# Kernel tuning notes

Measured on AMD Instinct MI355X. Metric: run time of the kernel, lower is better.

Reference implementation:

```python
import jax, jax.numpy as jnp
import numpy as np

THRESH = 1.0
TAU_M = 20.0
TAU_S = 5.0
NUM_STEPS = 16
SCALE = 0.3
BATCH = 128
DM = float(np.exp(-1.0 / TAU_M))  # membrane decay per step
DS = float(np.exp(-1.0 / TAU_S))  # synaptic decay per step


@jax.custom_vjp
def spike_fn(u):
    # Heaviside spike with rectangular surrogate gradient.
    return (u > 0.0).astype(u.dtype)

def _spike_fwd(u):
    return (u > 0.0).astype(u.dtype), u

def _spike_bwd(u, g):
    return (g * (jnp.abs(u) < 0.5).astype(u.dtype),)

spike_fn.defvjp(_spike_fwd, _spike_bwd)


def _conv(x, w):
    # 5x5, stride 1, pad 2, no bias (NCHW / OIHW)
    return jax.lax.conv_general_dilated(x, w, (1, 1), ((2, 2), (2, 2)),
                                        dimension_numbers=('NCHW', 'OIHW', 'NCHW'))


def _noso(op, x, sav, vm, vs):
    # NOSO dual-time-constant neuron: u = sav * (op(vm) - op(vs));
    # sav gates the neuron off after its single spike.
    vm = vm * DM + x
    vs = vs * DS + x
    um = op(vm)
    us = op(vs)
    u = sav * (um - us)
    spike = spike_fn(u - THRESH)
    sav = sav * (1.0 - spike)
    return sav, vm, vs, um, u, spike


def _min_pool(spike, latency):
    # latency-based 2x2/stride-2 min-pool: pass the spike of the
    # earliest-firing (minimum-latency) neuron in each window.
    B, C, H, W = spike.shape
    s = spike.reshape(B, C, H // 2, 2, W // 2, 2)
    l = latency.reshape(B, C, H // 2, 2, W // 2, 2)
    lmin = jnp.min(l, axis=(3, 5), keepdims=True)
    return jnp.max(s * (l == lmin).astype(s.dtype), axis=(3, 5))


def _fmnist_forward(inp, w_conv1, w_conv2, w_fc1, w_fc2):
    B = inp.shape[0]
    f32 = jnp.float32
    x = inp * SCALE
    z = lambda *s: jnp.zeros(s, f32)
    o = lambda *s: jnp.ones(s, f32)
    carry = (
        z(B, 1, 28, 28), z(B, 1, 28, 28),                      # input_u, in_spike
        z(B, 1, 28, 28), z(B, 1, 28, 28), o(B, 32, 28, 28),    # hc1_vm, hc1_vs, hc1_sav
        z(B, 32, 28, 28), NUM_STEPS * o(B, 32, 28, 28),        # p1_te, p1_lat
        z(B, 32, 14, 14), z(B, 32, 14, 14), o(B, 64, 14, 14),  # hc2_vm, hc2_vs, hc2_sav
        z(B, 64, 14, 14), NUM_STEPS * o(B, 64, 14, 14),        # p2_te, p2_lat
        z(B, 3136), z(B, 3136), o(B, 600),                     # hf1_vm, hf1_vs, hf1_sav
        z(B, 600), z(B, 600), o(B, 10),                        # hf2_vm, hf2_vs, hf2_sav
        NUM_STEPS * o(B, 10), z(B, 10), z(B, 10),              # out_t, out_u, t_elapse
        jnp.zeros(5, f32),                                     # sum_sp
    )

    def step(c, _):
        (input_u, in_spike, hc1_vm, hc1_vs, hc1_sav, p1_te, p1_lat,
         hc2_vm, hc2_vs, hc2_sav, p2_te, p2_lat,
         hf1_vm, hf1_vs, hf1_sav, hf2_vm, hf2_vs, hf2_sav,
         out_t, out_u, t_el, sum_sp) = c
        sg = jax.lax.stop_gradient
        # input encoding neuron (leaky integrator with reset-by-spike, thresh=1.0)
        input_u = input_u * DM * (1.0 - in_spike) + x
        in_spike = spike_fn(input_u - 1.0)
        # conv layer 1
        hc1_sav, hc1_vm, hc1_vs, hc1_um, _, hc1_spike = _noso(
            lambda v: _conv(v, w_conv1), in_spike, hc1_sav, hc1_vm, hc1_vs)
        p1_te = p1_te + sg(((p1_te + (hc1_um != 0).astype(jnp.float32)) != 0).astype(jnp.float32))
        p1_lat = p1_lat + sg(hc1_spike * (p1_te - NUM_STEPS + 1.0))
        # conv layer 2 on latency min-pooled spikes
        hc2_in = _min_pool(hc1_spike, sg(p1_lat))
        hc2_sav, hc2_vm, hc2_vs, hc2_um, _, hc2_spike = _noso(
            lambda v: _conv(v, w_conv2), hc2_in, hc2_sav, hc2_vm, hc2_vs)
        p2_te = p2_te + sg(((p2_te + (hc2_um != 0).astype(jnp.float32)) != 0).astype(jnp.float32))
        p2_lat = p2_lat + sg(hc2_spike * (p2_te - NUM_STEPS + 1.0))
        # fc layer 1
        hf1_in = _min_pool(hc2_spike, sg(p2_lat)).reshape(B, -1)
        hf1_sav, hf1_vm, hf1_vs, _, _, hf1_spike = _noso(
            lambda v: v @ w_fc1.T, hf1_in, hf1_sav, hf1_vm, hf1_vs)
        # output fc layer (outneuron=True: also exposes u)
        hf2_sav, hf2_vm, hf2_vs, _, hf2_u, hf2_spike = _noso(
            lambda v: v @ w_fc2.T, hf1_spike, hf2_sav, hf2_vm, hf2_vs)
        t_el = t_el + sg(((t_el + (hf2_u != 0).astype(jnp.float32)) != 0).astype(jnp.float32))
        out_t = out_t + hf2_spike * sg(t_el - NUM_STEPS)  # dodt forward: spike latency
        out_u = out_u + hf2_spike * hf2_u
        sum_sp = sum_sp + sg(jnp.stack([in_spike.sum(), hc1_spike.sum(), hc2_spike.sum(),
                                        hf1_spike.sum(), hf2_spike.sum()]))
        return (input_u, in_spike, hc1_vm, hc1_vs, hc1_sav, p1_te, p1_lat,
                hc2_vm, hc2_vs, hc2_sav, p2_te, p2_lat,
                hf1_vm, hf1_vs, hf1_sav, hf2_vm, hf2_vs, hf2_sav,
                out_t, out_u, t_el, sum_sp), None

    c, _ = jax.lax.scan(step, carry, None, length=NUM_STEPS)
    out_t, out_u, sum_sp = c[-4], c[-3], c[-1]
    return out_t, out_u, sum_sp


def _xavier(key, shape, fan_in, fan_out):
    bound = float(np.sqrt(6.0 / (fan_in + fan_out)))
    return jax.random.uniform(key, shape, jnp.float32, -bound, bound)


def setup_inputs() -> dict:
    key = jax.random.key(0)
    k0, k1, k2, k3, k4 = jax.random.split(key, 5)
    return {
        "input": jax.random.uniform(k0, (BATCH, 1, 28, 28), jnp.float32),
        "w_conv1": _xavier(k1, (32, 1, 5, 5), 1 * 25, 32 * 25),
        "w_conv2": _xavier(k2, (64, 32, 5, 5), 32 * 25, 64 * 25),
        "w_fc1": _xavier(k3, (600, 3136), 3136, 600),
        "w_fc2": _xavier(k4, (10, 600), 600, 10),
        "batch_size": BATCH,
    }


def reference(input, w_conv1, w_conv2, w_fc1, w_fc2, batch_size):
    return _fmnist_forward(input, w_conv1, w_conv2, w_fc1, w_fc2)
```

## Files before the change

### kernel.cpp

```cpp
#include <hip/hip_runtime.h>

#define BATCH 128

constexpr float DM = 0.95122942450071400910f;
constexpr float DS = 0.81873075307798185867f;

constexpr size_t o_wt   = 0;
constexpr size_t o_inb  = o_wt  + (size_t)3136 * 600;
constexpr size_t o_p1b  = o_inb + (size_t)16 * 128 * 32;
constexpr size_t o_flag = o_p1b + (size_t)16 * 128 * 32 * 18;
constexpr size_t o_p2m  = o_flag + 2048;
constexpr size_t o_c1   = o_p2m + 200704;
constexpr size_t TOTALF = o_c1 + (size_t)16 * 128 * 600 + 16;

__device__ __forceinline__ void block_sum_atomic(float v, float* red, float* dst) {
    int lane = threadIdx.x & 63;
    int wid  = threadIdx.x >> 6;
    #pragma unroll
    for (int o = 32; o; o >>= 1) v += __shfl_down(v, o, 64);
    if (lane == 0) red[wid] = v;
    __syncthreads();
    if (threadIdx.x == 0) {
        int nw = ((int)blockDim.x + 63) >> 6;
        float t = 0.f;
        for (int w = 0; w < nw; ++w) t += red[w];
        if (t != 0.f) atomicAdd(dst, t);
    }
    __syncthreads();
}

__global__ void k_transpose(const float* __restrict__ w, float* __restrict__ wt,
                            float* __restrict__ outz) {
    __shared__ float tile[32][33];
    int k0 = blockIdx.x * 32, j0 = blockIdx.y * 32;
    int lx = threadIdx.x & 31, ly = threadIdx.x >> 5;
    if (blockIdx.x == 0 && blockIdx.y == 0 && threadIdx.x < 5) outz[threadIdx.x] = 0.f;
    #pragma unroll
    for (int r = 0; r < 32; r += 8) {
        int j = j0 + ly + r, k = k0 + lx;
        tile[ly + r][lx] = (j < 600 && k < 3136) ? w[(size_t)j * 3136 + k] : 0.f;
    }
    __syncthreads();
    #pragma unroll
    for (int r = 0; r < 32; r += 8) {
        int k = k0 + ly + r, j = j0 + lx;
        if (k < 3136 && j < 600) wt[(size_t)k * 600 + j] = tile[lx][ly + r];
    }
}

__launch_bounds__(896)
__global__ void k_encode(const float* __restrict__ inp, unsigned* __restrict__ inb,
                         float* __restrict__ ssp) {
    __shared__ float red[16];
    int b = blockIdx.x, tid = threadIdx.x;
    int w = tid >> 6, lane = tid & 63;
    int r = lane >> 5, x = lane & 31;
    int y = 2 * w + r;
    float xv = (x < 28) ? inp[b * 784 + y * 28 + x] * 0.3f : 0.f;
    if (tid < 64) {
        int t = tid >> 2, rsel = tid & 3;
        inb[((size_t)t * 128 + b) * 32 + (rsel < 2 ? rsel : 28 + rsel)] = 0u;
    }
    float uin = 0.f, isp = 0.f, cnt = 0.f;
    for (int t = 0; t < 16; ++t) {
        uin = uin * DM * (1.f - isp) + xv;
        isp = (uin > 1.f && x < 28) ? 1.f : 0.f;
        cnt += isp;
        unsigned long long m = __ballot(isp != 0.f);
        if (lane == 0)       inb[((size_t)t * 128 + b) * 32 + (2 * w + 2)] = ((unsigned)m) << 2;
        else if (lane == 32) inb[((size_t)t * 128 + b) * 32 + (2 * w + 3)] = ((unsigned)(m >> 32)) << 2;
    }
    block_sum_atomic(cnt, red, &ssp[0]);
}

__launch_bounds__(256)
__global__ void k_conv1(const float* __restrict__ w1, const unsigned* __restrict__ inb,
                        unsigned* __restrict__ p1b, unsigned short* __restrict__ flags,
                        float* __restrict__ ssp) {
    __shared__ float2 lutA[320];
    __shared__ float2 lutB[320];
    __shared__ unsigned sib[512];
    __shared__ unsigned wor[8];
    __shared__ unsigned s_tm[4];
    __shared__ float red[4];
    int bo = blockIdx.x, b = bo >> 4, op = bo & 15;
    int oc0 = op * 2;
    int tid = threadIdx.x;
    int px = tid & 15, py = tid >> 4;
    bool pv = (px < 14) && (py < 14);
    int pb = (py < 14) ? 2 * py : 0;

    if (tid < 128) {
        int t = tid >> 3, k = tid & 7;
        int oc = oc0 + (k >> 2), rsel = k & 3;
        p1b[(((size_t)t * 128 + b) * 32 + oc) * 18 + (rsel < 2 ? rsel : 14 + rsel)] = 0u;
    }
    for (int e = tid; e < 320; e += 256) {
        int ky = e >> 6, m = e & 63;
        const float* wA = w1 + oc0 * 25 + ky * 5;
        float a0 = 0.f, a1 = 0.f, b0 = 0.f, b1 = 0.f;
        #pragma unroll
        for (int kx = 0; kx < 5; ++kx) {
            if ((m >> kx) & 1)       { a0 += wA[kx]; b0 += wA[25 + kx]; }
            if ((m >> (kx + 1)) & 1) { a1 += wA[kx]; b1 += wA[25 + kx]; }
        }
        lutA[e] = make_float2(a0, a1);
        lutB[e] = make_float2(b0, b1);
    }
    unsigned lb = 0;
    {
        unsigned w0 = inb[((size_t)(tid >> 5) * 128 + b) * 32 + (tid & 31)];
        unsigned w1v = inb[((size_t)((tid + 256) >> 5) * 128 + b) * 32 + (tid & 31)];
        sib[tid] = w0;
        sib[tid + 256] = w1v;
        if (w0)  lb |= 1u << (tid >> 5);
        if (w1v) lb |= 1u << ((tid >> 5) + 8);
    }
    #pragma unroll
    for (int off = 32; off; off >>= 1) lb |= __shfl_xor(lb, off, 64);
    if ((tid & 63) == 0) s_tm[tid >> 6] = lb;
    if (tid < 8) wor[tid] = 0u;
    __syncthreads();

    unsigned tmask = s_tm[0] | s_tm[1] | s_tm[2] | s_tm[3];
    unsigned smask = tmask;
    smask |= smask << 1; smask |= smask << 2; smask |= smask << 4; smask |= smask << 8;

    float umA[2][2] = {}, usA[2][2] = {}, teA[2][2] = {};
    float savA[2][2] = {{1.f,1.f},{1.f,1.f}}, ltA[2][2] = {{16.f,16.f},{16.f,16.f}};
    float umB[2][2] = {}, usB[2][2] = {}, teB[2][2] = {};
    float savB[2][2] = {{1.f,1.f},{1.f,1.f}}, ltB[2][2] = {{16.f,16.f},{16.f,16.f}};
    unsigned pmA = 0, pmB = 0;

    for (int t = 0; t < 16; ++t) {
        if (!((smask >> t) & 1u)) continue;
        unsigned rw[6];
        #pragma unroll
        for (int j = 0; j < 6; ++j) rw[j] = sib[t * 32 + pb + j];
        unsigned orall = rw[0] | rw[1] | rw[2] | rw[3] | rw[4] | rw[5];

        float cA[2][2] = {}, cB[2][2] = {};
        if (orall) {
            unsigned sh[6];
            #pragma unroll
            for (int j = 0; j < 6; ++j) sh[j] = (rw[j] >> (2 * px)) & 63u;
            #pragma unroll
            for (int r = 0; r < 2; ++r)
                #pragma unroll
                for (int ky = 0; ky < 5; ++ky) {
                    unsigned idx = ky * 64 + sh[r + ky];
                    float2 vA = lutA[idx];
                    float2 vB = lutB[idx];
                    cA[r][0] += vA.x; cA[r][1] += vA.y;
                    cB[r][0] += vB.x; cB[r][1] += vB.y;
                }
        }
        float sA[2][2], sB[2][2];
        #pragma unroll
        for (int r = 0; r < 2; ++r)
            #pragma unroll
            for (int cc = 0; cc < 2; ++cc) {
                umA[r][cc] = fmaf(umA[r][cc], DM, cA[r][cc]);
                usA[r][cc] = fmaf(usA[r][cc], DS, cA[r][cc]);
                float uA = savA[r][cc] * (umA[r][cc] - usA[r][cc]);
                bool fA = uA > 1.f;
                float a = fA ? 1.f : 0.f;
                savA[r][cc] = fA ? 0.f : savA[r][cc];
                teA[r][cc] += ((teA[r][cc] != 0.f) || (umA[r][cc] != 0.f)) ? 1.f : 0.f;
                ltA[r][cc] += a * (teA[r][cc] - 15.f);
                sA[r][cc] = a;
                umB[r][cc] = fmaf(umB[r][cc], DM, cB[r][cc]);
                usB[r][cc] = fmaf(usB[r][cc], DS, cB[r][cc]);
                float uB = savB[r][cc] * (umB[r][cc] - usB[r][cc]);
                bool fB = uB > 1.f;
                float bb = fB ? 1.f : 0.f;
                savB[r][cc] = fB ? 0.f : savB[r][cc];
                teB[r][cc] += ((teB[r][cc] != 0.f) || (umB[r][cc] != 0.f)) ? 1.f : 0.f;
                ltB[r][cc] += bb * (teB[r][cc] - 15.f);
                sB[r][cc] = bb;
            }
        float sany = sA[0][0] + sA[0][1] + sA[1][0] + sA[1][1]
                   + sB[0][0] + sB[0][1] + sB[1][0] + sB[1][1];
        if (!__any(pv && sany != 0.f)) continue;
        float lmA = fminf(fminf(ltA[0][0], ltA[0][1]), fminf(ltA[1][0], ltA[1][1]));
        float oA = fmaxf(fmaxf(ltA[0][0] == lmA ? sA[0][0] : 0.f, ltA[0][1] == lmA ? sA[0][1] : 0.f),
                         fmaxf(ltA[1][0] == lmA ? sA[1][0] : 0.f, ltA[1][1] == lmA ? sA[1][1] : 0.f));
        float lmB = fminf(fminf(ltB[0][0], ltB[0][1]), fminf(ltB[1][0], ltB[1][1]));
        float oB = fmaxf(fmaxf(ltB[0][0] == lmB ? sB[0][0] : 0.f, ltB[0][1] == lmB ? sB[0][1] : 0.f),
                         fmaxf(ltB[1][0] == lmB ? sB[1][0] : 0.f, ltB[1][1] == lmB ? sB[1][1] : 0.f));
        bool hitA = (oA != 0.f) && pv;
        bool hitB = (oB != 0.f) && pv;
        unsigned long long balA = __ballot(hitA);
        unsigned long long balB = __ballot(hitB);
        int k = tid & 63;
        if (k < 4) {
            int prow = (tid >> 6) * 4 + k;
            if (prow < 14) {
                unsigned wdA = ((unsigned)(balA >> (k * 16)) & 0x3FFFu) << 2;
                unsigned wdB = ((unsigned)(balB >> (k * 16)) & 0x3FFFu) << 2;
                p1b[(((size_t)t * 128 + b) * 32 + oc0)     * 18 + prow + 2] = wdA;
                p1b[(((size_t)t * 128 + b) * 32 + oc0 + 1) * 18 + prow + 2] = wdB;
            }
        }
        if (hitA) pmA |= 1u << t;
        if (hitB) pmB |= 1u << t;
    }

    unsigned pA = pmA, pB = pmB;
    #pragma unroll
    for (int off = 32; off; off >>= 1) {
        pA |= __shfl_xor(pA, off, 64);
        pB |= __shfl_xor(pB, off, 64);
    }
    if ((tid & 63) == 0) { wor[(tid >> 6) * 2] = pA; wor[(tid >> 6) * 2 + 1] = pB; }
    float cnt = 0.f;
    if (pv)
        cnt = 8.f - (savA[0][0] + savA[0][1] + savA[1][0] + savA[1][1]
                   + savB[0][0] + savB[0][1] + savB[1][0] + savB[1][1]);
    block_sum_atomic(cnt, red, &ssp[1]);
    if (tid == 0) {
        flags[b * 32 + oc0]     = (unsigned short)(wor[0] | wor[2] | wor[4] | wor[6]);
        flags[b * 32 + oc0 + 1] = (unsigned short)(wor[1] | wor[3] | wor[5] | wor[7]);
    }
}

__launch_bounds__(256)
__global__ void k_conv2(const float* __restrict__ w2, const unsigned* __restrict__ p1b,
                        const unsigned short* __restrict__ flags,
                        unsigned short* __restrict__ p2m, float* __restrict__ ssp) {
    __shared__ float2 lut2[5120];
    int bo = blockIdx.x, op = bo & 31, bq = bo >> 5;
    int oc0 = op * 2;
    int tid = threadIdx.x;
    int wv = tid >> 6, lane = tid & 63;
    int b = bq * 4 + wv;
    bool valid = lane < 49;
    int pr = valid ? (lane / 7) : 0;
    int pc = valid ? (lane - pr * 7) : 0;
    int y0 = 2 * pr, x0 = 2 * pc;

    for (int e = tid; e < 5120; e += 256) {
        int m = e & 31, icky = e >> 5;
        const float* wA = w2 + oc0 * 800 + icky * 5;
        float a = 0.f, c = 0.f;
        #pragma unroll
        for (int kx = 0; kx < 5; ++kx)
            if ((m >> kx) & 1) { a += wA[kx]; c += wA[800 + kx]; }
        lut2[e] = make_float2(a, c);
    }
    unsigned fl = flags[b * 32 + (lane & 31)];
    __syncthreads();

    float umA[2][2] = {}, usA[2][2] = {}, teA[2][2] = {};
    float savA[2][2] = {{1.f,1.f},{1.f,1.f}}, ltA[2][2] = {{16.f,16.f},{16.f,16.f}};
    float umB[2][2] = {}, usB[2][2] = {}, teB[2][2] = {};
    float savB[2][2] = {{1.f,1.f},{1.f,1.f}}, ltB[2][2] = {{16.f,16.f},{16.f,16.f}};
    unsigned pmA = 0, pmB = 0;
    bool started = false;

    for (int t = 0; t < 16; ++t) {
        unsigned actbm = (unsigned)__ballot(((fl >> t) & 1u) && (lane < 32));
        started = started || (actbm != 0);
        if (!started) continue;
        float cA[2][2] = {}, cB[2][2] = {};
        unsigned bm = actbm;
        while (bm) {
            int ic = __builtin_ctz(bm); bm &= bm - 1;
            const unsigned* rp = p1b + (((size_t)t * 128 + b) * 32 + ic) * 18 + y0;
            unsigned r0 = rp[0], r1 = rp[1], r2 = rp[2],
                     r3 = rp[3], r4 = rp[4], r5 = rp[5];
            unsigned orall = r0 | r1 | r2 | r3 | r4 | r5;
            if (!valid || ((orall >> x0) & 63u) == 0) continue;
            unsigned sh[6] = {r0 >> x0, r1 >> x0, r2 >> x0, r3 >> x0, r4 >> x0, r5 >> x0};
            int base = ic * 160;
            #pragma unroll
            for (int r = 0; r < 2; ++r)
                #pragma unroll
                for (int ky = 0; ky < 5; ++ky) {
                    unsigned s6 = sh[r + ky];
                    float2 v0 = lut2[base + ky * 32 + (s6 & 31u)];
                    float2 v1 = lut2[base + ky * 32 + ((s6 >> 1) & 31u)];
                    cA[r][0] += v0.x; cB[r][0] += v0.y;
                    cA[r][1] += v1.x; cB[r][1] += v1.y;
                }
        }
        float sA[2][2], sB[2][2];
        #pragma unroll
        for (int r = 0; r < 2; ++r)
            #pragma unroll
            for (int cc = 0; cc < 2; ++cc) {
                umA[r][cc] = fmaf(umA[r][cc], DM, cA[r][cc]);
                usA[r][cc] = fmaf(usA[r][cc], DS, cA[r][cc]);
                float uA = savA[r][cc] * (umA[r][cc] - usA[r][cc]);
                bool fA = uA > 1.f;
                float a = fA ? 1.f : 0.f;
                savA[r][cc] = fA ? 0.f : savA[r][cc];
                teA[r][cc] += ((teA[r][cc] != 0.f) || (umA[r][cc] != 0.f)) ? 1.f : 0.f;
                ltA[r][cc] += a * (teA[r][cc] - 15.f);
                sA[r][cc] = a;
                umB[r][cc] = fmaf(umB[r][cc], DM, cB[r][cc]);
                usB[r][cc] = fmaf(usB[r][cc], DS, cB[r][cc]);
                float uB = savB[r][cc] * (umB[r][cc] - usB[r][cc]);
                bool fB = uB > 1.f;
                float bb = fB ? 1.f : 0.f;
                savB[r][cc] = fB ? 0.f : savB[r][cc];
                teB[r][cc] += ((teB[r][cc] != 0.f) || (umB[r][cc] != 0.f)) ? 1.f : 0.f;
                ltB[r][cc] += bb * (teB[r][cc] - 15.f);
                sB[r][cc] = bb;
            }
        float sany = sA[0][0] + sA[0][1] + sA[1][0] + sA[1][1]
                   + sB[0][0] + sB[0][1] + sB[1][0] + sB[1][1];
        if (!__any(valid && sany != 0.f)) continue;
        float lmA = fminf(fminf(ltA[0][0], ltA[0][1]), fminf(ltA[1][0], ltA[1][1]));
        float oA = fmaxf(fmaxf(ltA[0][0] == lmA ? sA[0][0] : 0.f, ltA[0][1] == lmA ? sA[0][1] : 0.f),
                         fmaxf(ltA[1][0] == lmA ? sA[1][0] : 0.f, ltA[1][1] == lmA ? sA[1][1] : 0.f));
        float lmB = fminf(fminf(ltB[0][0], ltB[0][1]), fminf(ltB[1][0], ltB[1][1]));
        float oB = fmaxf(fmaxf(ltB[0][0] == lmB ? sB[0][0] : 0.f, ltB[0][1] == lmB ? sB[0][1] : 0.f),
                         fmaxf(ltB[1][0] == lmB ? sB[1][0] : 0.f, ltB[1][1] == lmB ? sB[1][1] : 0.f));
        if (valid && oA != 0.f) pmA |= 1u << t;
        if (valid && oB != 0.f) pmB |= 1u << t;
    }
    if (valid) {
        int pos = pr * 7 + pc;
        p2m[((size_t)b * 64 + oc0)     * 49 + pos] = (unsigned short)pmA;
        p2m[((size_t)b * 64 + oc0 + 1) * 49 + pos] = (unsigned short)pmB;
    }
    float cnt = 0.f;
    if (valid)
        cnt = 8.f - (savA[0][0] + savA[0][1] + savA[1][0] + savA[1][1]
                   + savB[0][0] + savB[0][1] + savB[1][0] + savB[1][1]);
    __syncthreads();
    block_sum_atomic(cnt, (float*)lut2, &ssp[2]);
}

__launch_bounds__(640)
__global__ void k_fc1pre(const float* __restrict__ wt, const unsigned short* __restrict__ p2m,
                         float* __restrict__ C1) {
    __shared__ unsigned short s_m[3136];
    __shared__ int s_idx[3136];
    __shared__ int s_nnz;
    int bt = blockIdx.x;
    int b = bt & 127, t = bt >> 7;
    int tid = threadIdx.x;

    for (int k = tid; k < 3136; k += 640) s_m[k] = p2m[(size_t)b * 3136 + k];
    __syncthreads();
    if (tid < 64) {
        int count = 0;
        for (int o = 0; o < 64; ++o) {
            unsigned v = (tid < 49) ? (unsigned)s_m[o * 49 + tid] : 0u;
            unsigned long long m = __ballot((v >> t) & 1u);
            if ((m >> tid) & 1ull)
                s_idx[count + __popcll(m & ((1ull << tid) - 1ull))] = o * 49 + tid;
            count += __popcll(m);
        }
        if (tid == 0) s_nnz = count;
    }
    __syncthreads();
    int nnz = s_nnz;

    if (tid < 600) {
        float a0 = 0.f, a1 = 0.f, a2 = 0.f, a3 = 0.f;
        int i = 0;
        for (; i + 4 <= nnz; i += 4) {
            a0 += wt[(size_t)s_idx[i]     * 600 + tid];
            a1 += wt[(size_t)s_idx[i + 1] * 600 + tid];
            a2 += wt[(size_t)s_idx[i + 2] * 600 + tid];
            a3 += wt[(size_t)s_idx[i + 3] * 600 + tid];
        }
        for (; i < nnz; ++i) a0 += wt[(size_t)s_idx[i] * 600 + tid];
        C1[(size_t)bt * 600 + tid] = (a0 + a1) + (a2 + a3);
    }
}

__launch_bounds__(640)
__global__ void k_fc12b(const float* __restrict__ C1, const float* __restrict__ wf2,
                        float* __restrict__ out) {
    __shared__ unsigned short s_m1[600];
    __shared__ float red[16];
    __shared__ float s_c2[10];
    int b = blockIdx.x, tid = threadIdx.x;
    int w = tid >> 6, lane = tid & 63;

    float cnt1 = 0.f;
    if (tid < 600) {
        float c[16];
        #pragma unroll
        for (int t = 0; t < 16; ++t) c[t] = C1[((size_t)t * 128 + b) * 600 + tid];
        float um = 0.f, us = 0.f, sv = 1.f;
        unsigned msk = 0;
        #pragma unroll
        for (int t = 0; t < 16; ++t) {
            um = fmaf(um, DM, c[t]);
            us = fmaf(us, DS, c[t]);
            float u = sv * (um - us);
            float s = (u > 1.f) ? 1.f : 0.f;
            sv *= (1.f - s);
            msk |= (s != 0.f) ? (1u << t) : 0u;
            cnt1 += s;
        }
        s_m1[tid] = (unsigned short)msk;
    }
    block_sum_atomic(cnt1, red, &out[2563]);

    const float* wrow = wf2 + w * 600;
    float wv[10]; unsigned mv[10];
    #pragma unroll
    for (int i = 0; i < 10; ++i) {
        int j = lane + i * 64;
        bool ok = (j < 600);
        wv[i] = ok ? wrow[j] : 0.f;
        mv[i] = ok ? (unsigned)s_m1[j] : 0u;
    }
    float f2um = 0.f, f2us = 0.f, f2sv = 1.f;
    float tel = 0.f, ot = 16.f, ou = 0.f, cnt2 = 0.f;
    for (int t = 0; t < 16; ++t) {
        float a = 0.f;
        #pragma unroll
        for (int i = 0; i < 10; ++i) a += ((mv[i] >> t) & 1u) ? wv[i] : 0.f;
        #pragma unroll
        for (int o = 32; o; o >>= 1) a += __shfl_down(a, o, 64);
        if (lane == 0) {
            f2um = fmaf(f2um, DM, a);
            f2us = fmaf(f2us, DS, a);
            float u = f2sv * (f2um - f2us);
            float s2 = (u > 1.f) ? 1.f : 0.f;
            f2sv *= (1.f - s2);
            tel += ((tel != 0.f) || (u != 0.f)) ? 1.f : 0.f;
            ot += s2 * (tel - 16.f);
            ou += s2 * u;
            cnt2 += s2;
        }
    }
    if (lane == 0) {
        out[b * 10 + w] = ot;
        out[1280 + b * 10 + w] = ou;
        s_c2[w] = cnt2;
    }
    __syncthreads();
    if (tid == 0) {
        float tt = 0.f;
        for (int j = 0; j < 10; ++j) tt += s_c2[j];
        if (tt != 0.f) atomicAdd(&out[2564], tt);
    }
}

extern "C" void kernel_launch(void* const* d_in, const int* in_sizes, int n_in,
                              void* d_out, int out_size, void* d_ws, size_t ws_size,
                              hipStream_t stream) {
    (void)in_sizes; (void)n_in; (void)out_size;
    if (ws_size < TOTALF * sizeof(float)) return;

    const float* inp = (const float*)d_in[0];
    const float* w1  = (const float*)d_in[1];
    const float* w2  = (const float*)d_in[2];
    const float* wf1 = (const float*)d_in[3];
    const float* wf2 = (const float*)d_in[4];
    float* ws  = (float*)d_ws;
    float* out = (float*)d_out;

    k_transpose<<<dim3(98, 19), 256, 0, stream>>>(wf1, ws + o_wt, out + 2560);

    k_encode<<<BATCH, 896, 0, stream>>>(inp, (unsigned*)(ws + o_inb), out + 2560);
    k_conv1<<<BATCH * 16, 256, 0, stream>>>(w1, (const unsigned*)(ws + o_inb),
                                            (unsigned*)(ws + o_p1b),
                                            (unsigned short*)(ws + o_flag), out + 2560);
    k_conv2<<<(BATCH / 4) * 32, 256, 0, stream>>>(w2, (const unsigned*)(ws + o_p1b),
                                                  (const unsigned short*)(ws + o_flag),
                                                  (unsigned short*)(ws + o_p2m), out + 2560);
    k_fc1pre<<<16 * BATCH, 640, 0, stream>>>(ws + o_wt, (const unsigned short*)(ws + o_p2m),
                                             ws + o_c1);
    k_fc12b<<<BATCH, 640, 0, stream>>>(ws + o_c1, wf2, out);
}
```

Baseline: 106.5 us.

## Fold weight transpose into conv1 grid and replace spike-count atomics with per-block partials

Removes the standalone transpose launch by appending the fc1 weight-transpose tiles as extra blocks of the conv1 grid, so the transpose runs alongside conv1 work. Spike-count atomics in encode/conv1/conv2 become per-block stores to a workspace array, reduced at the end by block 0 of the final kernel. The two conv1 LUTs are merged into one float4 table so each lookup is a single shared load. This saves one kernel launch and the atomic contention, but adds a serial tail reduction in block 0 of fc12b.

Measured after the change: 96.87 us. 1.1x faster.

```diff
diff --git a/kernel.cpp b/kernel.cpp
--- a/kernel.cpp
+++ b/kernel.cpp
@@ -11,7 +11,24 @@
 constexpr size_t o_flag = o_p1b + (size_t)16 * 128 * 32 * 18;
 constexpr size_t o_p2m  = o_flag + 2048;
 constexpr size_t o_c1   = o_p2m + 200704;
-constexpr size_t TOTALF = o_c1 + (size_t)16 * 128 * 600 + 16;
+constexpr size_t o_cnt  = o_c1 + (size_t)16 * 128 * 600;
+constexpr size_t TOTALF = o_cnt + 3200 + 16;
+
+__device__ __forceinline__ void block_sum_store(float v, float* red, float* dst) {
+    int lane = threadIdx.x & 63;
+    int wid  = threadIdx.x >> 6;
+    #pragma unroll
+    for (int o = 32; o; o >>= 1) v += __shfl_down(v, o, 64);
+    if (lane == 0) red[wid] = v;
+    __syncthreads();
+    if (threadIdx.x == 0) {
+        int nw = ((int)blockDim.x + 63) >> 6;
+        float t = 0.f;
+        for (int w = 0; w < nw; ++w) t += red[w];
+        *dst = t;
+    }
+    __syncthreads();
+}
 
 __device__ __forceinline__ void block_sum_atomic(float v, float* red, float* dst) {
     int lane = threadIdx.x & 63;
@@ -29,28 +46,9 @@
     __syncthreads();
 }
 
-__global__ void k_transpose(const float* __restrict__ w, float* __restrict__ wt,
-                            float* __restrict__ outz) {
-    __shared__ float tile[32][33];
-    int k0 = blockIdx.x * 32, j0 = blockIdx.y * 32;
-    int lx = threadIdx.x & 31, ly = threadIdx.x >> 5;
-    if (blockIdx.x == 0 && blockIdx.y == 0 && threadIdx.x < 5) outz[threadIdx.x] = 0.f;
-    #pragma unroll
-    for (int r = 0; r < 32; r += 8) {
-        int j = j0 + ly + r, k = k0 + lx;
-        tile[ly + r][lx] = (j < 600 && k < 3136) ? w[(size_t)j * 3136 + k] : 0.f;
-    }
-    __syncthreads();
-    #pragma unroll
-    for (int r = 0; r < 32; r += 8) {
-        int k = k0 + ly + r, j = j0 + lx;
-        if (k < 3136 && j < 600) wt[(size_t)k * 600 + j] = tile[lx][ly + r];
-    }
-}
-
 __launch_bounds__(896)
 __global__ void k_encode(const float* __restrict__ inp, unsigned* __restrict__ inb,
-                         float* __restrict__ ssp) {
+                         float* __restrict__ cnts) {
     __shared__ float red[16];
     int b = blockIdx.x, tid = threadIdx.x;
     int w = tid >> 6, lane = tid & 63;
@@ -70,22 +68,43 @@
         if (lane == 0)       inb[((size_t)t * 128 + b) * 32 + (2 * w + 2)] = ((unsigned)m) << 2;
         else if (lane == 32) inb[((size_t)t * 128 + b) * 32 + (2 * w + 3)] = ((unsigned)(m >> 32)) << 2;
     }
-    block_sum_atomic(cnt, red, &ssp[0]);
+    block_sum_store(cnt, red, &cnts[b]);
 }
 
 __launch_bounds__(256)
 __global__ void k_conv1(const float* __restrict__ w1, const unsigned* __restrict__ inb,
                         unsigned* __restrict__ p1b, unsigned short* __restrict__ flags,
-                        float* __restrict__ ssp) {
-    __shared__ float2 lutA[320];
-    __shared__ float2 lutB[320];
+                        const float* __restrict__ wf1, float* __restrict__ wt,
+                        float* __restrict__ cnts) {
+    __shared__ float4 lutbuf[320];
     __shared__ unsigned sib[512];
     __shared__ unsigned wor[8];
     __shared__ unsigned s_tm[4];
     __shared__ float red[4];
-    int bo = blockIdx.x, b = bo >> 4, op = bo & 15;
+    int bo = blockIdx.x;
+    int tid = threadIdx.x;
+
+    if (bo >= 2048) {
+        float* tile = (float*)lutbuf;
+        int bx = bo - 2048;
+        int k0 = (bx % 98) * 32, j0 = (bx / 98) * 32;
+        int lx = tid & 31, ly = tid >> 5;
+        #pragma unroll
+        for (int r = 0; r < 32; r += 8) {
+            int j = j0 + ly + r, k = k0 + lx;
+            tile[(ly + r) * 33 + lx] = (j < 600 && k < 3136) ? wf1[(size_t)j * 3136 + k] : 0.f;
+        }
+        __syncthreads();
+        #pragma unroll
+        for (int r = 0; r < 32; r += 8) {
+            int k = k0 + ly + r, j = j0 + lx;
+            if (k < 3136 && j < 600) wt[(size_t)k * 600 + j] = tile[lx * 33 + ly + r];
+        }
+        return;
+    }
+
+    int b = bo >> 4, op = bo & 15;
     int oc0 = op * 2;
-    int tid = threadIdx.x;
     int px = tid & 15, py = tid >> 4;
     bool pv = (px < 14) && (py < 14);
     int pb = (py < 14) ? 2 * py : 0;
@@ -104,8 +123,7 @@
             if ((m >> kx) & 1)       { a0 += wA[kx]; b0 += wA[25 + kx]; }
             if ((m >> (kx + 1)) & 1) { a1 += wA[kx]; b1 += wA[25 + kx]; }
         }
-        lutA[e] = make_float2(a0, a1);
-        lutB[e] = make_float2(b0, b1);
+        lutbuf[e] = make_float4(a0, a1, b0, b1);
     }
     unsigned lb = 0;
     {
@@ -148,11 +166,9 @@
             for (int r = 0; r < 2; ++r)
                 #pragma unroll
                 for (int ky = 0; ky < 5; ++ky) {
-                    unsigned idx = ky * 64 + sh[r + ky];
-                    float2 vA = lutA[idx];
-                    float2 vB = lutB[idx];
-                    cA[r][0] += vA.x; cA[r][1] += vA.y;
-                    cB[r][0] += vB.x; cB[r][1] += vB.y;
+                    float4 v = lutbuf[ky * 64 + sh[r + ky]];
+                    cA[r][0] += v.x; cA[r][1] += v.y;
+                    cB[r][0] += v.z; cB[r][1] += v.w;
                 }
         }
         float sA[2][2], sB[2][2];
@@ -217,7 +233,7 @@
     if (pv)
         cnt = 8.f - (savA[0][0] + savA[0][1] + savA[1][0] + savA[1][1]
                    + savB[0][0] + savB[0][1] + savB[1][0] + savB[1][1]);
-    block_sum_atomic(cnt, red, &ssp[1]);
+    block_sum_store(cnt, red, &cnts[128 + bo]);
     if (tid == 0) {
         flags[b * 32 + oc0]     = (unsigned short)(wor[0] | wor[2] | wor[4] | wor[6]);
         flags[b * 32 + oc0 + 1] = (unsigned short)(wor[1] | wor[3] | wor[5] | wor[7]);
@@ -227,7 +243,7 @@
 __launch_bounds__(256)
 __global__ void k_conv2(const float* __restrict__ w2, const unsigned* __restrict__ p1b,
                         const unsigned short* __restrict__ flags,
-                        unsigned short* __restrict__ p2m, float* __restrict__ ssp) {
+                        unsigned short* __restrict__ p2m, float* __restrict__ cnts) {
     __shared__ float2 lut2[5120];
     int bo = blockIdx.x, op = bo & 31, bq = bo >> 5;
     int oc0 = op * 2;
@@ -330,18 +346,19 @@
         cnt = 8.f - (savA[0][0] + savA[0][1] + savA[1][0] + savA[1][1]
                    + savB[0][0] + savB[0][1] + savB[1][0] + savB[1][1]);
     __syncthreads();
-    block_sum_atomic(cnt, (float*)lut2, &ssp[2]);
+    block_sum_store(cnt, (float*)lut2, &cnts[2176 + bo]);
 }
 
 __launch_bounds__(640)
 __global__ void k_fc1pre(const float* __restrict__ wt, const unsigned short* __restrict__ p2m,
-                         float* __restrict__ C1) {
+                         float* __restrict__ C1, float* __restrict__ out) {
     __shared__ unsigned short s_m[3136];
     __shared__ int s_idx[3136];
     __shared__ int s_nnz;
     int bt = blockIdx.x;
     int b = bt & 127, t = bt >> 7;
     int tid = threadIdx.x;
+    if (bt == 0 && tid < 2) out[2563 + tid] = 0.f;
 
     for (int k = tid; k < 3136; k += 640) s_m[k] = p2m[(size_t)b * 3136 + k];
     __syncthreads();
@@ -375,7 +392,7 @@
 
 __launch_bounds__(640)
 __global__ void k_fc12b(const float* __restrict__ C1, const float* __restrict__ wf2,
-                        float* __restrict__ out) {
+                        const float* __restrict__ cnts, float* __restrict__ out) {
     __shared__ unsigned short s_m1[600];
     __shared__ float red[16];
     __shared__ float s_c2[10];
@@ -443,6 +460,17 @@
         for (int j = 0; j < 10; ++j) tt += s_c2[j];
         if (tt != 0.f) atomicAdd(&out[2564], tt);
     }
+    if (b == 0) {
+        float v = 0.f;
+        for (int k = tid; k < 128; k += 640) v += cnts[k];
+        block_sum_store(v, red, &out[2560]);
+        v = 0.f;
+        for (int k = tid; k < 2048; k += 640) v += cnts[128 + k];
+        block_sum_store(v, red, &out[2561]);
+        v = 0.f;
+        for (int k = tid; k < 1024; k += 640) v += cnts[2176 + k];
+        block_sum_store(v, red, &out[2562]);
+    }
 }
 
 extern "C" void kernel_launch(void* const* d_in, const int* in_sizes, int n_in,
@@ -459,16 +487,15 @@
     float* ws  = (float*)d_ws;
     float* out = (float*)d_out;
 
-    k_transpose<<<dim3(98, 19), 256, 0, stream>>>(wf1, ws + o_wt, out + 2560);
-
-    k_encode<<<BATCH, 896, 0, stream>>>(inp, (unsigned*)(ws + o_inb), out + 2560);
-    k_conv1<<<BATCH * 16, 256, 0, stream>>>(w1, (const unsigned*)(ws + o_inb),
-                                            (unsigned*)(ws + o_p1b),
-                                            (unsigned short*)(ws + o_flag), out + 2560);
+    k_encode<<<BATCH, 896, 0, stream>>>(inp, (unsigned*)(ws + o_inb), ws + o_cnt);
+    k_conv1<<<2048 + 1862, 256, 0, stream>>>(w1, (const unsigned*)(ws + o_inb),
+                                             (unsigned*)(ws + o_p1b),
+                                             (unsigned short*)(ws + o_flag),
+                                             wf1, ws + o_wt, ws + o_cnt);
     k_conv2<<<(BATCH / 4) * 32, 256, 0, stream>>>(w2, (const unsigned*)(ws + o_p1b),
                                                   (const unsigned short*)(ws + o_flag),
-                                                  (unsigned short*)(ws + o_p2m), out + 2560);
+                                                  (unsigned short*)(ws + o_p2m), ws + o_cnt);
     k_fc1pre<<<16 * BATCH, 640, 0, stream>>>(ws + o_wt, (const unsigned short*)(ws + o_p2m),
-                                             ws + o_c1);
-    k_fc12b<<<BATCH, 640, 0, stream>>>(ws + o_c1, wf2, out);
-}
+                                             ws + o_c1, out);
+    k_fc12b<<<BATCH, 640, 0, stream>>>(ws + o_c1, wf2, ws + o_cnt, out);
+}
```
